# Kernel optimization log

Measured on AMD Instinct MI355X. Metric: run time of the kernel, lower is better.

The kernel has to match this reference:

```python
import jax, jax.numpy as jnp
import numpy as np

N, E, B = 50000, 800000, 64
IN, H, OUT = 64, 128, 64


def _gcn_norm(edge_index, num_nodes):
    # PyG gcn_norm with add_self_loops=True: A_hat = A + I, norm = d^-1/2[src]*d^-1/2[dst]
    loop = jnp.arange(num_nodes)
    src = jnp.concatenate([edge_index[0], loop])
    dst = jnp.concatenate([edge_index[1], loop])
    deg = jax.ops.segment_sum(jnp.ones_like(dst, dtype=jnp.float32), dst,
                              num_segments=num_nodes)  # >= 1 due to self-loops
    dis = deg ** -0.5
    norm = dis[src] * dis[dst]  # [E+N]
    return src, dst, norm


def _gcn_layer(x, W, b, src, dst, norm, num_nodes):
    h = x @ W                                   # linear first (GCNConv order)
    msg = h[src] * norm[:, None]                # gather + normalize, [E+N, H]
    out = jax.ops.segment_sum(msg, dst, num_segments=num_nodes)  # scatter-add
    return out + b


def setup_inputs() -> dict:
    key = jax.random.key(0)
    ks = jax.random.split(key, 12)
    x = jax.random.normal(ks[0], (N, IN), dtype=jnp.float32)
    edge_index = jax.random.randint(ks[1], (2, E), 0, N, dtype=jnp.int64)
    batch = jnp.sort(jax.random.randint(ks[2], (N,), 0, B, dtype=jnp.int64))

    def lin(k, fan_in, fan_out):
        s = 1.0 / np.sqrt(fan_in)
        return jax.random.uniform(k, (fan_in, fan_out), jnp.float32, -s, s)

    return {
        "x": x, "edge_index": edge_index, "batch": batch,
        "W1": lin(ks[3], IN, H), "b1": jnp.zeros((H,), jnp.float32),
        "W2": lin(ks[4], H, H),  "b2": jnp.zeros((H,), jnp.float32),
        "W3": lin(ks[5], H, H),  "b3": jnp.zeros((H,), jnp.float32),
        "W4": lin(ks[6], H, OUT), "b4": jnp.zeros((OUT,), jnp.float32),
    }


def reference(x, edge_index, batch, W1, b1, W2, b2, W3, b3, W4, b4):
    src, dst, norm = _gcn_norm(edge_index, N)
    h = jax.nn.relu(_gcn_layer(x, W1, b1, src, dst, norm, N))
    h = jax.nn.relu(_gcn_layer(h, W2, b2, src, dst, norm, N))
    # global mean pool over graphs
    sums = jax.ops.segment_sum(h, batch, num_segments=B)          # [B, H]
    cnts = jax.ops.segment_sum(jnp.ones((N,), jnp.float32), batch, num_segments=B)
    pooled = sums / jnp.maximum(cnts, 1.0)[:, None]
    # MLP head
    return jax.nn.relu(pooled @ W3 + b3) @ W4 + b4                # [B, OUT]
```

## Files before the change

kernel.cpp:

```cpp
#include <hip/hip_runtime.h>


__device__ __forceinline__ float ldf(const void* p, long long i, int f32) {
    if (f32) return ((const float*)p)[i];
    unsigned int u = ((const unsigned short*)p)[i];
    return __uint_as_float(u << 16);
}
__device__ __forceinline__ float bfl(unsigned int u) { return __uint_as_float(u << 16); }
__device__ __forceinline__ float bfh(unsigned int u) { return __uint_as_float(u & 0xFFFF0000u); }
__device__ __forceinline__ int ld_idx(const int* p, long long i, int i64) {
    return i64 ? p[2 * i] : p[i];
}
__device__ __forceinline__ unsigned short f2bf(float v) {
    unsigned int x = __float_as_uint(v);
    return (unsigned short)((x + 0x7FFFu + ((x >> 16) & 1u)) >> 16);
}
__device__ __forceinline__ int clampi(int v, int lo, int hi) {
    return v < lo ? lo : (v > hi ? hi : v);
}

#define OW1 0
#define OB1 8192
#define OW2 8320
#define OB2 24704
#define OW3 24832
#define OB3 41216
#define OW4 41344
#define OB4 49536
#define OTOT 49600


__global__ void gnn_prep(const void* W1, const void* b1, const void* W2, const void* b2,
                         const void* W3, const void* b3, const void* W4, const void* b4,
                         const int* __restrict__ ei,
                         int* __restrict__ flags_out,
                         int* __restrict__ degcnt, float* __restrict__ pooled,
                         float* __restrict__ wsW, int N, int B) {
    __shared__ int s_cnt, s_or;
    const int t = threadIdx.x;
    if (t == 0) { s_cnt = 0; s_or = 0; }
    __syncthreads();
    {
        const unsigned int* w1w = (const unsigned int*)W1;
        int c = 0, o = 0;
        for (int i = t; i < 512; i += 256) {
            unsigned int e = (w1w[i] >> 7) & 0xFFu;
            if (e >= 100 && e <= 140) c++;
        }
        for (int i = t; i < 1024; i += 256) o |= ei[2 * i + 1];
        atomicAdd(&s_cnt, c);
        atomicOr(&s_or, o);
    }
    __syncthreads();
    const int f32 = (s_cnt > 256) ? 0 : 1;
    if (blockIdx.x == 0 && t == 0) {
        flags_out[0] = f32;
        flags_out[1] = (s_or == 0) ? 1 : 0;
    }
    const int i = blockIdx.x * 256 + t;
    const int stride = gridDim.x * 256;
    for (int j = i; j < N; j += stride) degcnt[j] = 0;
    for (int j = i; j < B * 128; j += stride) pooled[j] = 0.f;
    for (int j = i; j < OTOT; j += stride) {
        float v;
        if      (j < OB1) v = ldf(W1, j - OW1, f32);
        else if (j < OW2) v = ldf(b1, j - OB1, f32);
        else if (j < OB2) v = ldf(W2, j - OW2, f32);
        else if (j < OW3) v = ldf(b2, j - OB2, f32);
        else if (j < OB3) v = ldf(W3, j - OW3, f32);
        else if (j < OW4) v = ldf(b3, j - OB3, f32);
        else if (j < OB4) v = ldf(W4, j - OW4, f32);
        else              v = ldf(b4, j - OB4, f32);
        wsW[j] = v;
    }
}


__global__ void gnn_hist(const int* __restrict__ ei, int E, int N,
                         const int* __restrict__ flags, int* __restrict__ degcnt,
                         int* __restrict__ rank) {
    int base = (blockIdx.x * 256 + threadIdx.x) * 4;
    if (base >= E) return;
    int i64 = flags[1];
    int m = min(4, E - base);
    int d[4], r[4];
#pragma unroll
    for (int j = 0; j < 4; ++j)
        if (j < m) d[j] = clampi(ld_idx(ei, (long long)E + base + j, i64), 0, N - 1);
#pragma unroll
    for (int j = 0; j < 4; ++j)
        if (j < m) r[j] = atomicAdd(&degcnt[d[j]], 1);
#pragma unroll
    for (int j = 0; j < 4; ++j)
        if (j < m) rank[base + j] = r[j];
}

__global__ void gnn_scan1(const int* __restrict__ cnt, int* __restrict__ excl,
                          int* __restrict__ sums, float* __restrict__ dis, int N) {
    __shared__ int sh[256];
    int t = threadIdx.x;
    int i = blockIdx.x * 256 + t;
    int v = (i < N) ? cnt[i] : 0;
    sh[t] = v;
    __syncthreads();
    for (int off = 1; off < 256; off <<= 1) {
        int a = (t >= off) ? sh[t - off] : 0;
        __syncthreads();
        sh[t] += a;
        __syncthreads();
    }
    if (i < N) {
        excl[i] = sh[t] - v;
        dis[i] = rsqrtf((float)v + 1.0f);
    }
    if (t == 255) sums[blockIdx.x] = sh[255];
}

__global__ void gnn_scan2(int* __restrict__ sums, int nb) {
    __shared__ int sh[256];
    int t = threadIdx.x;
    int v = (t < nb) ? sums[t] : 0;
    sh[t] = v;
    __syncthreads();
    for (int off = 1; off < 256; off <<= 1) {
        int a = (t >= off) ? sh[t - off] : 0;
        __syncthreads();
        sh[t] += a;
        __syncthreads();
    }
    if (t < nb) sums[t] = sh[t] - v;
}

template <bool SMALLN>
__global__ void gnn_fill(const int* __restrict__ ei, const int* __restrict__ excl,
                         const int* __restrict__ bsums, const int* __restrict__ rank,
                         void* __restrict__ csr, int E, int N,
                         const int* __restrict__ flags,
                         const void* __restrict__ x, const float* __restrict__ dis,
                         unsigned short* __restrict__ xb) {
    const int tid = blockIdx.x * 256 + threadIdx.x;
    const int i64 = flags[1];
    if (tid < E) {
        int s = clampi(ld_idx(ei, (long long)tid, i64), 0, N - 1);
        int d = clampi(ld_idx(ei, (long long)E + tid, i64), 0, N - 1);
        int pos = excl[d] + bsums[d >> 8] + rank[tid];
        if (SMALLN) ((unsigned short*)csr)[pos] = (unsigned short)s;
        else        ((int*)csr)[pos] = s;
    }
    const int f32 = flags[0];
    const int total = N * 16;
    const int stride = gridDim.x * 256;
    for (int j = tid; j < total; j += stride) {
        int n = j >> 4;
        float dn = dis[n];
        float v0, v1, v2, v3;
        if (f32) {
            float4 xv = ((const float4*)x)[j];
            v0 = xv.x; v1 = xv.y; v2 = xv.z; v3 = xv.w;
        } else {
            ushort4 xv = ((const ushort4*)x)[j];
            v0 = bfl(xv.x); v1 = bfl(xv.y); v2 = bfl(xv.z); v3 = bfl(xv.w);
        }
        ushort4 o;
        o.x = f2bf(v0 * dn); o.y = f2bf(v1 * dn);
        o.z = f2bf(v2 * dn); o.w = f2bf(v3 * dn);
        ((ushort4*)xb)[j] = o;
    }
}

template <bool SMALLN>
__device__ __forceinline__ int csr_at(const void* csr, int e) {
    return SMALLN ? (int)((const unsigned short*)csr)[e] : ((const int*)csr)[e];
}


template <bool SMALLN>
__global__ __launch_bounds__(256) void gnn_l1l2(const unsigned short* __restrict__ xb,
                                                const int* __restrict__ excl,
                                                const int* __restrict__ bsums,
                                                const void* __restrict__ csr,
                                                const float* __restrict__ dis,
                                                const float* __restrict__ W1,
                                                const float* __restrict__ b1,
                                                const float* __restrict__ W2,
                                                int N, int E,
                                                unsigned short* __restrict__ A2) {
    __shared__ float Xs[16 * 68];
    __shared__ float Hs[16 * 128];
    const int t = threadIdx.x;
    const int nbase = blockIdx.x * 16;
    const int nd = t >> 4;
    const int eslot = (t >> 3) & 1;
    const int fg = t & 7;
    const int n = nbase + nd;

    float a0 = 0.f, a1 = 0.f, a2 = 0.f, a3 = 0.f;
    float a4 = 0.f, a5 = 0.f, a6 = 0.f, a7 = 0.f;
    if (n < N) {
        if (eslot == 1) {
            uint4 us = *(const uint4*)(xb + (long long)n * 64 + fg * 8);
            a0 = bfl(us.x); a1 = bfh(us.x); a2 = bfl(us.y); a3 = bfh(us.y);
            a4 = bfl(us.z); a5 = bfh(us.z); a6 = bfl(us.w); a7 = bfh(us.w);
        }
        int beg = excl[n] + bsums[n >> 8];
        int end = (n + 1 < N) ? (excl[n + 1] + bsums[(n + 1) >> 8]) : E;
        int e = beg + eslot;
        for (; e + 6 < end; e += 8) {
            int s0 = csr_at<SMALLN>(csr, e),     s1 = csr_at<SMALLN>(csr, e + 2);
            int s2 = csr_at<SMALLN>(csr, e + 4), s3 = csr_at<SMALLN>(csr, e + 6);
            uint4 u0 = *(const uint4*)(xb + (long long)s0 * 64 + fg * 8);
            uint4 u1 = *(const uint4*)(xb + (long long)s1 * 64 + fg * 8);
            uint4 u2 = *(const uint4*)(xb + (long long)s2 * 64 + fg * 8);
            uint4 u3 = *(const uint4*)(xb + (long long)s3 * 64 + fg * 8);
            a0 += bfl(u0.x); a1 += bfh(u0.x); a2 += bfl(u0.y); a3 += bfh(u0.y);
            a4 += bfl(u0.z); a5 += bfh(u0.z); a6 += bfl(u0.w); a7 += bfh(u0.w);
            a0 += bfl(u1.x); a1 += bfh(u1.x); a2 += bfl(u1.y); a3 += bfh(u1.y);
            a4 += bfl(u1.z); a5 += bfh(u1.z); a6 += bfl(u1.w); a7 += bfh(u1.w);
            a0 += bfl(u2.x); a1 += bfh(u2.x); a2 += bfl(u2.y); a3 += bfh(u2.y);
            a4 += bfl(u2.z); a5 += bfh(u2.z); a6 += bfl(u2.w); a7 += bfh(u2.w);
            a0 += bfl(u3.x); a1 += bfh(u3.x); a2 += bfl(u3.y); a3 += bfh(u3.y);
            a4 += bfl(u3.z); a5 += bfh(u3.z); a6 += bfl(u3.w); a7 += bfh(u3.w);
        }
        for (; e < end; e += 2) {
            int s = csr_at<SMALLN>(csr, e);
            uint4 u = *(const uint4*)(xb + (long long)s * 64 + fg * 8);
            a0 += bfl(u.x); a1 += bfh(u.x); a2 += bfl(u.y); a3 += bfh(u.y);
            a4 += bfl(u.z); a5 += bfh(u.z); a6 += bfl(u.w); a7 += bfh(u.w);
        }
    }
    a0 += __shfl_xor(a0, 8); a1 += __shfl_xor(a1, 8);
    a2 += __shfl_xor(a2, 8); a3 += __shfl_xor(a3, 8);
    a4 += __shfl_xor(a4, 8); a5 += __shfl_xor(a5, 8);
    a6 += __shfl_xor(a6, 8); a7 += __shfl_xor(a7, 8);
    if (eslot == 0) {
        const float dn = (n < N) ? dis[n] : 0.f;
        float4 o0, o1;
        o0.x = a0 * dn; o0.y = a1 * dn; o0.z = a2 * dn; o0.w = a3 * dn;
        o1.x = a4 * dn; o1.y = a5 * dn; o1.z = a6 * dn; o1.w = a7 * dn;
        *(float4*)&Xs[nd * 68 + fg * 8]     = o0;
        *(float4*)&Xs[nd * 68 + fg * 8 + 4] = o1;
    }
    __syncthreads();

    const int fgB = t & 31, ng = t >> 5;
    const int f0 = fgB * 4, n0 = ng * 2;
    {
        const float4* Wp = (const float4*)W1;
        float4 acc[2];
#pragma unroll
        for (int j = 0; j < 2; ++j) acc[j] = make_float4(0.f, 0.f, 0.f, 0.f);
#pragma unroll 4
        for (int k4 = 0; k4 < 16; ++k4) {
            const float4 wa = Wp[(4 * k4 + 0) * 32 + fgB];
            const float4 wb = Wp[(4 * k4 + 1) * 32 + fgB];
            const float4 wc = Wp[(4 * k4 + 2) * 32 + fgB];
            const float4 wd = Wp[(4 * k4 + 3) * 32 + fgB];
#pragma unroll
            for (int j = 0; j < 2; ++j) {
                const float4 xv = *(const float4*)&Xs[(n0 + j) * 68 + k4 * 4];
                acc[j].x = fmaf(xv.x, wa.x, acc[j].x); acc[j].y = fmaf(xv.x, wa.y, acc[j].y);
                acc[j].z = fmaf(xv.x, wa.z, acc[j].z); acc[j].w = fmaf(xv.x, wa.w, acc[j].w);
                acc[j].x = fmaf(xv.y, wb.x, acc[j].x); acc[j].y = fmaf(xv.y, wb.y, acc[j].y);
                acc[j].z = fmaf(xv.y, wb.z, acc[j].z); acc[j].w = fmaf(xv.y, wb.w, acc[j].w);
                acc[j].x = fmaf(xv.z, wc.x, acc[j].x); acc[j].y = fmaf(xv.z, wc.y, acc[j].y);
                acc[j].z = fmaf(xv.z, wc.z, acc[j].z); acc[j].w = fmaf(xv.z, wc.w, acc[j].w);
                acc[j].x = fmaf(xv.w, wd.x, acc[j].x); acc[j].y = fmaf(xv.w, wd.y, acc[j].y);
                acc[j].z = fmaf(xv.w, wd.z, acc[j].z); acc[j].w = fmaf(xv.w, wd.w, acc[j].w);
            }
        }
        const float4 b = *(const float4*)&b1[f0];
#pragma unroll
        for (int j = 0; j < 2; ++j) {
            float4 a = acc[j];
            a.x = fmaxf(a.x + b.x, 0.f);
            a.y = fmaxf(a.y + b.y, 0.f);
            a.z = fmaxf(a.z + b.z, 0.f);
            a.w = fmaxf(a.w + b.w, 0.f);
            *(float4*)&Hs[(n0 + j) * 128 + f0] = a;
        }
    }
    __syncthreads();
    {
        const float4* Wp = (const float4*)W2;
        float4 acc[2];
#pragma unroll
        for (int j = 0; j < 2; ++j) acc[j] = make_float4(0.f, 0.f, 0.f, 0.f);
#pragma unroll 4
        for (int k4 = 0; k4 < 32; ++k4) {
            const float4 wa = Wp[(4 * k4 + 0) * 32 + fgB];
            const float4 wb = Wp[(4 * k4 + 1) * 32 + fgB];
            const float4 wc = Wp[(4 * k4 + 2) * 32 + fgB];
            const float4 wd = Wp[(4 * k4 + 3) * 32 + fgB];
#pragma unroll
            for (int j = 0; j < 2; ++j) {
                const float4 xv = *(const float4*)&Hs[(n0 + j) * 128 + k4 * 4];
                acc[j].x = fmaf(xv.x, wa.x, acc[j].x); acc[j].y = fmaf(xv.x, wa.y, acc[j].y);
                acc[j].z = fmaf(xv.x, wa.z, acc[j].z); acc[j].w = fmaf(xv.x, wa.w, acc[j].w);
                acc[j].x = fmaf(xv.y, wb.x, acc[j].x); acc[j].y = fmaf(xv.y, wb.y, acc[j].y);
                acc[j].z = fmaf(xv.y, wb.z, acc[j].z); acc[j].w = fmaf(xv.y, wb.w, acc[j].w);
                acc[j].x = fmaf(xv.z, wc.x, acc[j].x); acc[j].y = fmaf(xv.z, wc.y, acc[j].y);
                acc[j].z = fmaf(xv.z, wc.z, acc[j].z); acc[j].w = fmaf(xv.z, wc.w, acc[j].w);
                acc[j].x = fmaf(xv.w, wd.x, acc[j].x); acc[j].y = fmaf(xv.w, wd.y, acc[j].y);
                acc[j].z = fmaf(xv.w, wd.z, acc[j].z); acc[j].w = fmaf(xv.w, wd.w, acc[j].w);
            }
        }
#pragma unroll
        for (int j = 0; j < 2; ++j) {
            int nn = nbase + n0 + j;
            if (nn >= N) continue;
            const float dn = dis[nn];
            float4 a = acc[j];
            a.x *= dn; a.y *= dn; a.z *= dn; a.w *= dn;
            uint2 u;
            u.x = (unsigned int)f2bf(a.x) | ((unsigned int)f2bf(a.y) << 16);
            u.y = (unsigned int)f2bf(a.z) | ((unsigned int)f2bf(a.w) << 16);
            *(uint2*)(A2 + (long long)nn * 128 + f0) = u;
        }
    }
}


template <bool SMALLN>
__global__ __launch_bounds__(256) void gnn_agg_bf(const unsigned short* __restrict__ A2,
                                                  const int* __restrict__ excl,
                                                  const int* __restrict__ bsums,
                                                  const void* __restrict__ csr,
                                                  const float* __restrict__ dis,
                                                  const float* __restrict__ bias,
                                                  float* __restrict__ outC, int N, int E) {
    const int t = threadIdx.x;
    const int lane = t & 63;
    const int n = blockIdx.x * 4 + (t >> 6);
    const int eslot = lane >> 4;
    const int fg = lane & 15;
    float a0 = 0.f, a1 = 0.f, a2 = 0.f, a3 = 0.f;
    float a4 = 0.f, a5 = 0.f, a6 = 0.f, a7 = 0.f;
    if (n < N) {
        if (eslot == 3) {
            uint4 us = *(const uint4*)(A2 + (long long)n * 128 + fg * 8);
            a0 = bfl(us.x); a1 = bfh(us.x); a2 = bfl(us.y); a3 = bfh(us.y);
            a4 = bfl(us.z); a5 = bfh(us.z); a6 = bfl(us.w); a7 = bfh(us.w);
        }
        int beg = excl[n] + bsums[n >> 8];
        int end = (n + 1 < N) ? (excl[n + 1] + bsums[(n + 1) >> 8]) : E;
        int e = beg + eslot;
        for (; e + 12 < end; e += 16) {
            int s0 = csr_at<SMALLN>(csr, e),     s1 = csr_at<SMALLN>(csr, e + 4);
            int s2 = csr_at<SMALLN>(csr, e + 8), s3 = csr_at<SMALLN>(csr, e + 12);
            uint4 u0 = *(const uint4*)(A2 + (long long)s0 * 128 + fg * 8);
            uint4 u1 = *(const uint4*)(A2 + (long long)s1 * 128 + fg * 8);
            uint4 u2 = *(const uint4*)(A2 + (long long)s2 * 128 + fg * 8);
            uint4 u3 = *(const uint4*)(A2 + (long long)s3 * 128 + fg * 8);
            a0 += bfl(u0.x); a1 += bfh(u0.x); a2 += bfl(u0.y); a3 += bfh(u0.y);
            a4 += bfl(u0.z); a5 += bfh(u0.z); a6 += bfl(u0.w); a7 += bfh(u0.w);
            a0 += bfl(u1.x); a1 += bfh(u1.x); a2 += bfl(u1.y); a3 += bfh(u1.y);
            a4 += bfl(u1.z); a5 += bfh(u1.z); a6 += bfl(u1.w); a7 += bfh(u1.w);
            a0 += bfl(u2.x); a1 += bfh(u2.x); a2 += bfl(u2.y); a3 += bfh(u2.y);
            a4 += bfl(u2.z); a5 += bfh(u2.z); a6 += bfl(u2.w); a7 += bfh(u2.w);
            a0 += bfl(u3.x); a1 += bfh(u3.x); a2 += bfl(u3.y); a3 += bfh(u3.y);
            a4 += bfl(u3.z); a5 += bfh(u3.z); a6 += bfl(u3.w); a7 += bfh(u3.w);
        }
        for (; e < end; e += 4) {
            int s = csr_at<SMALLN>(csr, e);
            uint4 u = *(const uint4*)(A2 + (long long)s * 128 + fg * 8);
            a0 += bfl(u.x); a1 += bfh(u.x); a2 += bfl(u.y); a3 += bfh(u.y);
            a4 += bfl(u.z); a5 += bfh(u.z); a6 += bfl(u.w); a7 += bfh(u.w);
        }
    }
#pragma unroll
    for (int m = 16; m <= 32; m <<= 1) {
        a0 += __shfl_xor(a0, m); a1 += __shfl_xor(a1, m);
        a2 += __shfl_xor(a2, m); a3 += __shfl_xor(a3, m);
        a4 += __shfl_xor(a4, m); a5 += __shfl_xor(a5, m);
        a6 += __shfl_xor(a6, m); a7 += __shfl_xor(a7, m);
    }
    if (n < N && eslot == 0) {
        const float dn = dis[n];
        const float4 bA = *(const float4*)&bias[fg * 8];
        const float4 bB = *(const float4*)&bias[fg * 8 + 4];
        float4 o0, o1;
        o0.x = fmaxf(a0 * dn + bA.x, 0.f);
        o0.y = fmaxf(a1 * dn + bA.y, 0.f);
        o0.z = fmaxf(a2 * dn + bA.z, 0.f);
        o0.w = fmaxf(a3 * dn + bA.w, 0.f);
        o1.x = fmaxf(a4 * dn + bB.x, 0.f);
        o1.y = fmaxf(a5 * dn + bB.y, 0.f);
        o1.z = fmaxf(a6 * dn + bB.z, 0.f);
        o1.w = fmaxf(a7 * dn + bB.w, 0.f);
        *(float4*)(outC + (long long)n * 128 + fg * 8)     = o0;
        *(float4*)(outC + (long long)n * 128 + fg * 8 + 4) = o1;
    }
}


#define PSTRIP 32
__global__ __launch_bounds__(128) void gnn_pool(const float* __restrict__ h,
                                                const int* __restrict__ batch,
                                                const int* __restrict__ flags,
                                                float* __restrict__ pooled, int N, int B) {
    int i64 = flags[1];
    int f = threadIdx.x;
    int n0 = blockIdx.x * PSTRIP;
    if (n0 >= N) return;
    int nend = min(n0 + PSTRIP, N);
    int cur = clampi(ld_idx(batch, n0, i64), 0, B - 1);
    float acc = 0.0f;
    for (int n = n0; n < nend; ++n) {
        int b = clampi(ld_idx(batch, n, i64), 0, B - 1);
        if (b != cur) {
            atomicAdd(&pooled[cur * 128 + f], acc);
            acc = 0.0f; cur = b;
        }
        acc += h[(long long)n * 128 + f];
    }
    atomicAdd(&pooled[cur * 128 + f], acc);
}


__global__ __launch_bounds__(128) void gnn_head(const float* __restrict__ pooled,
                                                const int* __restrict__ batch,
                                                const float* __restrict__ W3,
                                                const float* __restrict__ b3,
                                                const float* __restrict__ W4,
                                                const float* __restrict__ b4,
                                                const int* __restrict__ flags,
                                                void* __restrict__ outv, int N) {
    __shared__ float xs[128];
    __shared__ float rs[128];
    __shared__ float cinv;
    int b = blockIdx.x, f = threadIdx.x;
    if (f == 0) {
        int i64 = flags[1];
        int L = 0, R = N;
        while (L < R) { int m = (L + R) >> 1; if (ld_idx(batch, m, i64) < b) L = m + 1; else R = m; }
        int lo = L;
        L = 0; R = N;
        while (L < R) { int m = (L + R) >> 1; if (ld_idx(batch, m, i64) < b + 1) L = m + 1; else R = m; }
        cinv = 1.0f / fmaxf((float)(L - lo), 1.0f);
    }
    __syncthreads();
    xs[f] = pooled[b * 128 + f] * cinv;
    __syncthreads();
    float acc = b3[f];
    for (int k = 0; k < 128; ++k) acc = fmaf(xs[k], W3[k * 128 + f], acc);
    rs[f] = fmaxf(acc, 0.f);
    __syncthreads();
    if (f < 64) {
        float a2 = b4[f];
        for (int k = 0; k < 128; ++k) a2 = fmaf(rs[k], W4[k * 64 + f], a2);
        if (flags[0]) ((float*)outv)[b * 64 + f] = a2;
        else          ((unsigned short*)outv)[b * 64 + f] = f2bf(a2);
    }
}


extern "C" void kernel_launch(void* const* d_in, const int* in_sizes, int n_in,
                              void* d_out, int out_size, void* d_ws, size_t ws_size,
                              hipStream_t stream) {
    const void* x  = d_in[0];
    const int* ei  = (const int*)d_in[1];
    const int* bat = (const int*)d_in[2];

    const int N = in_sizes[0] / 64;
    const int E = in_sizes[1] / 2;
    const int B = out_size / 64;
    const bool smalln = (N < 65536);

    char* p = (char*)d_ws;
    auto alloc = [&](size_t bytes) { void* q = (void*)p; p += (bytes + 255) & ~(size_t)255; return q; };
    int*   flags    = (int*)alloc(256);
    float* wsW      = (float*)alloc((size_t)OTOT * 4);
    int*   degcnt   = (int*)alloc((size_t)N * 4);
    float* dis      = (float*)alloc((size_t)N * 4);
    int*   excl     = (int*)alloc((size_t)N * 4);
    int*   bsums    = (int*)alloc(1024);
    int*   rank     = (int*)alloc((size_t)E * 4);
    void*  csr      = alloc((size_t)E * (smalln ? 2 : 4));
    unsigned short* xb = (unsigned short*)alloc((size_t)N * 64 * 2);
    float* C2       = (float*)alloc((size_t)N * 128 * 4);
    unsigned short* A2 = (unsigned short*)alloc((size_t)N * 128 * 2);
    float* pooled   = (float*)alloc((size_t)B * 128 * 4);
    (void)ws_size; (void)n_in;

    const int nbN = (N + 255) / 256;

    gnn_prep<<<512, 256, 0, stream>>>(d_in[3], d_in[4], d_in[5], d_in[6],
                                      d_in[7], d_in[8], d_in[9], d_in[10],
                                      ei, flags, degcnt, pooled, wsW, N, B);

    gnn_hist<<<(E + 1023) / 1024, 256, 0, stream>>>(ei, E, N, flags, degcnt, rank);
    gnn_scan1<<<nbN, 256, 0, stream>>>(degcnt, excl, bsums, dis, N);
    gnn_scan2<<<1, 256, 0, stream>>>(bsums, nbN);
    if (smalln)
        gnn_fill<true><<<(E + 255) / 256, 256, 0, stream>>>(ei, excl, bsums, rank, csr, E, N,
                                                            flags, x, dis, xb);
    else
        gnn_fill<false><<<(E + 255) / 256, 256, 0, stream>>>(ei, excl, bsums, rank, csr, E, N,
                                                             flags, x, dis, xb);

    const int nblk = (N + 15) / 16;

    if (smalln)
        gnn_l1l2<true><<<nblk, 256, 0, stream>>>(xb, excl, bsums, csr, dis,
                                                 wsW + OW1, wsW + OB1, wsW + OW2, N, E, A2);
    else
        gnn_l1l2<false><<<nblk, 256, 0, stream>>>(xb, excl, bsums, csr, dis,
                                                  wsW + OW1, wsW + OB1, wsW + OW2, N, E, A2);

    if (smalln)
        gnn_agg_bf<true><<<(N + 3) / 4, 256, 0, stream>>>(A2, excl, bsums, csr, dis,
                                                          wsW + OB2, C2, N, E);
    else
        gnn_agg_bf<false><<<(N + 3) / 4, 256, 0, stream>>>(A2, excl, bsums, csr, dis,
                                                           wsW + OB2, C2, N, E);

    gnn_pool<<<(N + PSTRIP - 1) / PSTRIP, 128, 0, stream>>>(C2, bat, flags, pooled, N, B);
    gnn_head<<<B, 128, 0, stream>>>(pooled, bat, wsW + OW3, wsW + OB3,
                                    wsW + OW4, wsW + OB4, flags, d_out, N);
}
```

Baseline: 284.9 us.

## Restructure gnn_l1l2 to 128 threads with 8-way edge split per node

The layer-1/2 fused kernel now runs 128 threads per block. Each wave processes one node per pass over 8 passes, splitting that node's edges eight ways across lanes and reducing them with three xor-shuffle stages. Each thread of the dense GEMM phase now computes 4 nodes instead of 2, which reuses each weight load across more rows. The layer-2 aggregation kernel drops its 4x manual unroll for a simple strided loop with an early exit. The aim is better load balance over variable-degree nodes, at the cost of less memory-level parallelism per lane and serialized passes.

Measured after the change: 290.5 us. Within noise of the previous version (+2.0%).

```diff
diff --git a/kernel.cpp b/kernel.cpp
--- a/kernel.cpp
+++ b/kernel.cpp
@@ -175,7 +175,7 @@
 
 
 template <bool SMALLN>
-__global__ __launch_bounds__(256) void gnn_l1l2(const unsigned short* __restrict__ xb,
+__global__ __launch_bounds__(128) void gnn_l1l2(const unsigned short* __restrict__ xb,
                                                 const int* __restrict__ excl,
                                                 const int* __restrict__ bsums,
                                                 const void* __restrict__ csr,
@@ -189,66 +189,58 @@
     __shared__ float Hs[16 * 128];
     const int t = threadIdx.x;
     const int nbase = blockIdx.x * 16;
-    const int nd = t >> 4;
-    const int eslot = (t >> 3) & 1;
-    const int fg = t & 7;
-    const int n = nbase + nd;
-
-    float a0 = 0.f, a1 = 0.f, a2 = 0.f, a3 = 0.f;
-    float a4 = 0.f, a5 = 0.f, a6 = 0.f, a7 = 0.f;
-    if (n < N) {
-        if (eslot == 1) {
-            uint4 us = *(const uint4*)(xb + (long long)n * 64 + fg * 8);
-            a0 = bfl(us.x); a1 = bfh(us.x); a2 = bfl(us.y); a3 = bfh(us.y);
-            a4 = bfl(us.z); a5 = bfh(us.z); a6 = bfl(us.w); a7 = bfh(us.w);
-        }
-        int beg = excl[n] + bsums[n >> 8];
-        int end = (n + 1 < N) ? (excl[n + 1] + bsums[(n + 1) >> 8]) : E;
-        int e = beg + eslot;
-        for (; e + 6 < end; e += 8) {
-            int s0 = csr_at<SMALLN>(csr, e),     s1 = csr_at<SMALLN>(csr, e + 2);
-            int s2 = csr_at<SMALLN>(csr, e + 4), s3 = csr_at<SMALLN>(csr, e + 6);
-            uint4 u0 = *(const uint4*)(xb + (long long)s0 * 64 + fg * 8);
-            uint4 u1 = *(const uint4*)(xb + (long long)s1 * 64 + fg * 8);
-            uint4 u2 = *(const uint4*)(xb + (long long)s2 * 64 + fg * 8);
-            uint4 u3 = *(const uint4*)(xb + (long long)s3 * 64 + fg * 8);
-            a0 += bfl(u0.x); a1 += bfh(u0.x); a2 += bfl(u0.y); a3 += bfh(u0.y);
-            a4 += bfl(u0.z); a5 += bfh(u0.z); a6 += bfl(u0.w); a7 += bfh(u0.w);
-            a0 += bfl(u1.x); a1 += bfh(u1.x); a2 += bfl(u1.y); a3 += bfh(u1.y);
-            a4 += bfl(u1.z); a5 += bfh(u1.z); a6 += bfl(u1.w); a7 += bfh(u1.w);
-            a0 += bfl(u2.x); a1 += bfh(u2.x); a2 += bfl(u2.y); a3 += bfh(u2.y);
-            a4 += bfl(u2.z); a5 += bfh(u2.z); a6 += bfl(u2.w); a7 += bfh(u2.w);
-            a0 += bfl(u3.x); a1 += bfh(u3.x); a2 += bfl(u3.y); a3 += bfh(u3.y);
-            a4 += bfl(u3.z); a5 += bfh(u3.z); a6 += bfl(u3.w); a7 += bfh(u3.w);
-        }
-        for (; e < end; e += 2) {
-            int s = csr_at<SMALLN>(csr, e);
-            uint4 u = *(const uint4*)(xb + (long long)s * 64 + fg * 8);
-            a0 += bfl(u.x); a1 += bfh(u.x); a2 += bfl(u.y); a3 += bfh(u.y);
-            a4 += bfl(u.z); a5 += bfh(u.z); a6 += bfl(u.w); a7 += bfh(u.w);
-        }
-    }
-    a0 += __shfl_xor(a0, 8); a1 += __shfl_xor(a1, 8);
-    a2 += __shfl_xor(a2, 8); a3 += __shfl_xor(a3, 8);
-    a4 += __shfl_xor(a4, 8); a5 += __shfl_xor(a5, 8);
-    a6 += __shfl_xor(a6, 8); a7 += __shfl_xor(a7, 8);
-    if (eslot == 0) {
-        const float dn = (n < N) ? dis[n] : 0.f;
-        float4 o0, o1;
-        o0.x = a0 * dn; o0.y = a1 * dn; o0.z = a2 * dn; o0.w = a3 * dn;
-        o1.x = a4 * dn; o1.y = a5 * dn; o1.z = a6 * dn; o1.w = a7 * dn;
-        *(float4*)&Xs[nd * 68 + fg * 8]     = o0;
-        *(float4*)&Xs[nd * 68 + fg * 8 + 4] = o1;
+    const int wave = t >> 6;
+    const int lane = t & 63;
+    const int eslot = lane >> 3;
+    const int fg = lane & 7;
+
+    for (int pass = 0; pass < 8; ++pass) {
+        const int ln = pass * 2 + wave;
+        const int n = nbase + ln;
+        float a0 = 0.f, a1 = 0.f, a2 = 0.f, a3 = 0.f;
+        float a4 = 0.f, a5 = 0.f, a6 = 0.f, a7 = 0.f;
+        if (n < N) {
+            if (eslot == 1) {
+                uint4 us = *(const uint4*)(xb + (long long)n * 64 + fg * 8);
+                a0 = bfl(us.x); a1 = bfh(us.x); a2 = bfl(us.y); a3 = bfh(us.y);
+                a4 = bfl(us.z); a5 = bfh(us.z); a6 = bfl(us.w); a7 = bfh(us.w);
+            }
+            int beg = excl[n] + bsums[n >> 8];
+            int end = (n + 1 < N) ? (excl[n + 1] + bsums[(n + 1) >> 8]) : E;
+            for (int e = beg + eslot; e < end; e += 8) {
+                int s = csr_at<SMALLN>(csr, e);
+                uint4 u = *(const uint4*)(xb + (long long)s * 64 + fg * 8);
+                a0 += bfl(u.x); a1 += bfh(u.x);
+                a2 += bfl(u.y); a3 += bfh(u.y);
+                a4 += bfl(u.z); a5 += bfh(u.z);
+                a6 += bfl(u.w); a7 += bfh(u.w);
+            }
+        }
+#pragma unroll
+        for (int m = 8; m <= 32; m <<= 1) {
+            a0 += __shfl_xor(a0, m); a1 += __shfl_xor(a1, m);
+            a2 += __shfl_xor(a2, m); a3 += __shfl_xor(a3, m);
+            a4 += __shfl_xor(a4, m); a5 += __shfl_xor(a5, m);
+            a6 += __shfl_xor(a6, m); a7 += __shfl_xor(a7, m);
+        }
+        if (eslot == 0) {
+            const float dn = (n < N) ? dis[n] : 0.f;
+            float4 o0, o1;
+            o0.x = a0 * dn; o0.y = a1 * dn; o0.z = a2 * dn; o0.w = a3 * dn;
+            o1.x = a4 * dn; o1.y = a5 * dn; o1.z = a6 * dn; o1.w = a7 * dn;
+            *(float4*)&Xs[ln * 68 + fg * 8]     = o0;
+            *(float4*)&Xs[ln * 68 + fg * 8 + 4] = o1;
+        }
     }
     __syncthreads();
 
     const int fgB = t & 31, ng = t >> 5;
-    const int f0 = fgB * 4, n0 = ng * 2;
+    const int f0 = fgB * 4, n0 = ng * 4;
     {
         const float4* Wp = (const float4*)W1;
-        float4 acc[2];
-#pragma unroll
-        for (int j = 0; j < 2; ++j) acc[j] = make_float4(0.f, 0.f, 0.f, 0.f);
+        float4 acc[4];
+#pragma unroll
+        for (int j = 0; j < 4; ++j) acc[j] = make_float4(0.f, 0.f, 0.f, 0.f);
 #pragma unroll 4
         for (int k4 = 0; k4 < 16; ++k4) {
             const float4 wa = Wp[(4 * k4 + 0) * 32 + fgB];
@@ -256,7 +248,7 @@
             const float4 wc = Wp[(4 * k4 + 2) * 32 + fgB];
             const float4 wd = Wp[(4 * k4 + 3) * 32 + fgB];
 #pragma unroll
-            for (int j = 0; j < 2; ++j) {
+            for (int j = 0; j < 4; ++j) {
                 const float4 xv = *(const float4*)&Xs[(n0 + j) * 68 + k4 * 4];
                 acc[j].x = fmaf(xv.x, wa.x, acc[j].x); acc[j].y = fmaf(xv.x, wa.y, acc[j].y);
                 acc[j].z = fmaf(xv.x, wa.z, acc[j].z); acc[j].w = fmaf(xv.x, wa.w, acc[j].w);
@@ -270,7 +262,7 @@
         }
         const float4 b = *(const float4*)&b1[f0];
 #pragma unroll
-        for (int j = 0; j < 2; ++j) {
+        for (int j = 0; j < 4; ++j) {
             float4 a = acc[j];
             a.x = fmaxf(a.x + b.x, 0.f);
             a.y = fmaxf(a.y + b.y, 0.f);
@@ -282,9 +274,9 @@
     __syncthreads();
     {
         const float4* Wp = (const float4*)W2;
-        float4 acc[2];
-#pragma unroll
-        for (int j = 0; j < 2; ++j) acc[j] = make_float4(0.f, 0.f, 0.f, 0.f);
+        float4 acc[4];
+#pragma unroll
+        for (int j = 0; j < 4; ++j) acc[j] = make_float4(0.f, 0.f, 0.f, 0.f);
 #pragma unroll 4
         for (int k4 = 0; k4 < 32; ++k4) {
             const float4 wa = Wp[(4 * k4 + 0) * 32 + fgB];
@@ -292,7 +284,7 @@
             const float4 wc = Wp[(4 * k4 + 2) * 32 + fgB];
             const float4 wd = Wp[(4 * k4 + 3) * 32 + fgB];
 #pragma unroll
-            for (int j = 0; j < 2; ++j) {
+            for (int j = 0; j < 4; ++j) {
                 const float4 xv = *(const float4*)&Hs[(n0 + j) * 128 + k4 * 4];
                 acc[j].x = fmaf(xv.x, wa.x, acc[j].x); acc[j].y = fmaf(xv.x, wa.y, acc[j].y);
                 acc[j].z = fmaf(xv.x, wa.z, acc[j].z); acc[j].w = fmaf(xv.x, wa.w, acc[j].w);
@@ -305,7 +297,7 @@
             }
         }
 #pragma unroll
-        for (int j = 0; j < 2; ++j) {
+        for (int j = 0; j < 4; ++j) {
             int nn = nbase + n0 + j;
             if (nn >= N) continue;
             const float dn = dis[nn];
@@ -331,41 +323,25 @@
     const int t = threadIdx.x;
     const int lane = t & 63;
     const int n = blockIdx.x * 4 + (t >> 6);
+    if (n >= N) return;
     const int eslot = lane >> 4;
     const int fg = lane & 15;
     float a0 = 0.f, a1 = 0.f, a2 = 0.f, a3 = 0.f;
     float a4 = 0.f, a5 = 0.f, a6 = 0.f, a7 = 0.f;
-    if (n < N) {
-        if (eslot == 3) {
-            uint4 us = *(const uint4*)(A2 + (long long)n * 128 + fg * 8);
-            a0 = bfl(us.x); a1 = bfh(us.x); a2 = bfl(us.y); a3 = bfh(us.y);
-            a4 = bfl(us.z); a5 = bfh(us.z); a6 = bfl(us.w); a7 = bfh(us.w);
-        }
-        int beg = excl[n] + bsums[n >> 8];
-        int end = (n + 1 < N) ? (excl[n + 1] + bsums[(n + 1) >> 8]) : E;
-        int e = beg + eslot;
-        for (; e + 12 < end; e += 16) {
-            int s0 = csr_at<SMALLN>(csr, e),     s1 = csr_at<SMALLN>(csr, e + 4);
-            int s2 = csr_at<SMALLN>(csr, e + 8), s3 = csr_at<SMALLN>(csr, e + 12);
-            uint4 u0 = *(const uint4*)(A2 + (long long)s0 * 128 + fg * 8);
-            uint4 u1 = *(const uint4*)(A2 + (long long)s1 * 128 + fg * 8);
-            uint4 u2 = *(const uint4*)(A2 + (long long)s2 * 128 + fg * 8);
-            uint4 u3 = *(const uint4*)(A2 + (long long)s3 * 128 + fg * 8);
-            a0 += bfl(u0.x); a1 += bfh(u0.x); a2 += bfl(u0.y); a3 += bfh(u0.y);
-            a4 += bfl(u0.z); a5 += bfh(u0.z); a6 += bfl(u0.w); a7 += bfh(u0.w);
-            a0 += bfl(u1.x); a1 += bfh(u1.x); a2 += bfl(u1.y); a3 += bfh(u1.y);
-            a4 += bfl(u1.z); a5 += bfh(u1.z); a6 += bfl(u1.w); a7 += bfh(u1.w);
-            a0 += bfl(u2.x); a1 += bfh(u2.x); a2 += bfl(u2.y); a3 += bfh(u2.y);
-            a4 += bfl(u2.z); a5 += bfh(u2.z); a6 += bfl(u2.w); a7 += bfh(u2.w);
-            a0 += bfl(u3.x); a1 += bfh(u3.x); a2 += bfl(u3.y); a3 += bfh(u3.y);
-            a4 += bfl(u3.z); a5 += bfh(u3.z); a6 += bfl(u3.w); a7 += bfh(u3.w);
-        }
-        for (; e < end; e += 4) {
-            int s = csr_at<SMALLN>(csr, e);
-            uint4 u = *(const uint4*)(A2 + (long long)s * 128 + fg * 8);
-            a0 += bfl(u.x); a1 += bfh(u.x); a2 += bfl(u.y); a3 += bfh(u.y);
-            a4 += bfl(u.z); a5 += bfh(u.z); a6 += bfl(u.w); a7 += bfh(u.w);
-        }
+    if (eslot == 3) {
+        uint4 us = *(const uint4*)(A2 + (long long)n * 128 + fg * 8);
+        a0 = bfl(us.x); a1 = bfh(us.x); a2 = bfl(us.y); a3 = bfh(us.y);
+        a4 = bfl(us.z); a5 = bfh(us.z); a6 = bfl(us.w); a7 = bfh(us.w);
+    }
+    int beg = excl[n] + bsums[n >> 8];
+    int end = (n + 1 < N) ? (excl[n + 1] + bsums[(n + 1) >> 8]) : E;
+    for (int e = beg + eslot; e < end; e += 4) {
+        int s = csr_at<SMALLN>(csr, e);
+        uint4 u = *(const uint4*)(A2 + (long long)s * 128 + fg * 8);
+        a0 += bfl(u.x); a1 += bfh(u.x);
+        a2 += bfl(u.y); a3 += bfh(u.y);
+        a4 += bfl(u.z); a5 += bfh(u.z);
+        a6 += bfl(u.w); a7 += bfh(u.w);
     }
 #pragma unroll
     for (int m = 16; m <= 32; m <<= 1) {
@@ -374,7 +350,7 @@
         a4 += __shfl_xor(a4, m); a5 += __shfl_xor(a5, m);
         a6 += __shfl_xor(a6, m); a7 += __shfl_xor(a7, m);
     }
-    if (n < N && eslot == 0) {
+    if (eslot == 0) {
         const float dn = dis[n];
         const float4 bA = *(const float4*)&bias[fg * 8];
         const float4 bB = *(const float4*)&bias[fg * 8 + 4];
@@ -501,10 +477,10 @@
     const int nblk = (N + 15) / 16;
 
     if (smalln)
-        gnn_l1l2<true><<<nblk, 256, 0, stream>>>(xb, excl, bsums, csr, dis,
+        gnn_l1l2<true><<<nblk, 128, 0, stream>>>(xb, excl, bsums, csr, dis,
                                                  wsW + OW1, wsW + OB1, wsW + OW2, N, E, A2);
     else
-        gnn_l1l2<false><<<nblk, 256, 0, stream>>>(xb, excl, bsums, csr, dis,
+        gnn_l1l2<false><<<nblk, 128, 0, stream>>>(xb, excl, bsums, csr, dis,
                                                   wsW + OW1, wsW + OB1, wsW + OW2, N, E, A2);
 
     if (smalln)
```
